# Performance work log

Measured on AMD Instinct MI355X. Metric: run time of the kernel, lower is better.

The kernel has to match this reference:

```python
import jax, jax.numpy as jnp
import numpy as np

EPS = 1e-5

def _batchnorm(h, gamma, beta):
    # training-mode BatchNorm1d over node dim, biased variance
    mu = jnp.mean(h, axis=0)
    var = jnp.mean((h - mu) ** 2, axis=0)
    return (h - mu) * jax.lax.rsqrt(var + EPS) * gamma + beta

def _sage(x, src, dst, n, Wl, b, Wr):
    # sum-aggregate source features into destinations, then linear + root linear
    agg = jax.ops.segment_sum(x[src], dst, num_segments=n)  # [N, F]
    return agg @ Wl + b + x @ Wr

def setup_inputs() -> dict:
    key = jax.random.key(0)
    ks = jax.random.split(key, 8)
    N, E, F, H, O = 200000, 1200000, 64, 128, 128
    s = lambda fan_in: 1.0 / np.sqrt(fan_in)
    return {
        "x": jax.random.normal(ks[0], (N, F), jnp.float32),
        "edge_index": jax.random.randint(ks[1], (2, E), 0, N, jnp.int64),
        "W1l": jax.random.normal(ks[2], (F, H), jnp.float32) * s(F),
        "b1": jnp.zeros((H,), jnp.float32),
        "W1r": jax.random.normal(ks[3], (F, H), jnp.float32) * s(F),
        "g1": jnp.ones((H,), jnp.float32),
        "be1": jnp.zeros((H,), jnp.float32),
        "W2l": jax.random.normal(ks[4], (H, O), jnp.float32) * s(H),
        "b2": jnp.zeros((O,), jnp.float32),
        "W2r": jax.random.normal(ks[5], (H, O), jnp.float32) * s(H),
        "g2": jnp.ones((O,), jnp.float32),
        "be2": jnp.zeros((O,), jnp.float32),
    }

def reference(x, edge_index, W1l, b1, W1r, g1, be1, W2l, b2, W2r, g2, be2):
    n = x.shape[0]
    src, dst = edge_index[0], edge_index[1]
    h = jax.nn.relu(_sage(x, src, dst, n, W1l, b1, W1r))
    h = _batchnorm(h, g1, be1)
    h = jax.nn.relu(_sage(h, src, dst, n, W2l, b2, W2r))
    h = _batchnorm(h, g2, be2)
    return jax.nn.relu(h)
```

## Files before the change

kernel.cpp:

```cpp
#include <hip/hip_runtime.h>

#define N_NODES 200000
#define N_EDGES 1200000
#define F_IN    64
#define F_H     128
#define BN_EPS  1e-5f

typedef short bf16x8 __attribute__((ext_vector_type(8)));
typedef float f32x4  __attribute__((ext_vector_type(4)));
typedef unsigned short us4 __attribute__((ext_vector_type(4)));

__device__ __forceinline__ unsigned short f2bf(float f) {
    union { float f; unsigned u; } v; v.f = f;
    unsigned r = (v.u + 0x7FFFu + ((v.u >> 16) & 1u)) >> 16;
    return (unsigned short)r;
}
__device__ __forceinline__ float bf2f(unsigned short b) {
    union { unsigned u; float f; } v; v.u = ((unsigned)b) << 16;
    return v.f;
}

__global__ void pack_weights_kernel(const float* __restrict__ W,
                                    const float* __restrict__ kscale,
                                    short* __restrict__ P, int KT)
{
    int t = blockIdx.x * 256 + threadIdx.x;
    if (t >= 8 * KT * 64) return;
    int lane = t & 63;
    int kt   = (t >> 6) % KT;
    int nt   = t / (64 * KT);
    int k0   = kt * 32 + (lane >> 4) * 8;
    int n    = nt * 16 + (lane & 15);
#pragma unroll
    for (int j = 0; j < 8; ++j) {
        float w = W[(size_t)(k0 + j) * 128 + n];
        if (kscale) w *= kscale[k0 + j];
        P[(size_t)t * 8 + j] = (short)f2bf(w);
    }
}

__global__ __launch_bounds__(256) void hist_kernel(const int* __restrict__ ei,
                                                   int* __restrict__ deg, int E)
{
    int e = blockIdx.x * 256 + threadIdx.x;
    if (e < E) atomicAdd(&deg[ei[E + e]], 1);
}

__global__ __launch_bounds__(256) void scan1_kernel(const int* __restrict__ deg,
        int* __restrict__ part, int* __restrict__ bsum, int n)
{
    __shared__ int s[256];
    int t = threadIdx.x;
    int base = blockIdx.x * 1024 + t * 4;
    int v[4];
#pragma unroll
    for (int j = 0; j < 4; ++j) v[j] = (base + j < n) ? deg[base + j] : 0;
    int tsum = v[0] + v[1] + v[2] + v[3];
    s[t] = tsum;
    __syncthreads();
    for (int off = 1; off < 256; off <<= 1) {
        int xv = (t >= off) ? s[t - off] : 0;
        __syncthreads();
        s[t] += xv;
        __syncthreads();
    }
    int excl = s[t] - tsum;
#pragma unroll
    for (int j = 0; j < 4; ++j) {
        if (base + j < n) part[base + j] = excl;
        excl += v[j];
    }
    if (t == 255) bsum[blockIdx.x] = s[255];
}

__global__ void scan2_kernel(int* __restrict__ bsum, int nb)
{
    __shared__ int s[256];
    int t = threadIdx.x;
    int v = (t < nb) ? bsum[t] : 0;
    s[t] = v;
    __syncthreads();
    for (int off = 1; off < 256; off <<= 1) {
        int xv = (t >= off) ? s[t - off] : 0;
        __syncthreads();
        s[t] += xv;
        __syncthreads();
    }
    if (t < nb) bsum[t] = s[t] - v;
}

__global__ __launch_bounds__(256) void scan3_kernel(
    const int* __restrict__ part, const int* __restrict__ bsum,
    const int* __restrict__ deg, int* __restrict__ rowptr,
    int* __restrict__ cursor, float* __restrict__ degf, int n, int E)
{
    int i = blockIdx.x * 256 + threadIdx.x;
    if (i == 0) rowptr[n] = E;
    if (i >= n) return;
    int r = part[i] + bsum[i >> 10];
    rowptr[i] = r;
    cursor[i] = r;
    degf[i]   = (float)deg[i];
}

__global__ __launch_bounds__(256) void fill_kernel(const int* __restrict__ ei,
        int* __restrict__ cursor, int* __restrict__ ssrc, int E)
{
    int e = blockIdx.x * 256 + threadIdx.x;
    if (e >= E) return;
    int d = ei[E + e];
    int pos = atomicAdd(&cursor[d], 1);
    ssrc[pos] = ei[e];
}

__global__ __launch_bounds__(256) void gather1_kernel(
    const float* __restrict__ x, const int* __restrict__ rowptr,
    const int* __restrict__ ssrc, unsigned short* __restrict__ aggb)
{
    const int tid  = threadIdx.x;
    const int wv   = tid >> 6;
    const int lane = tid & 63;
    const int sub  = lane >> 4;
    const int li   = lane & 15;
    const int row  = blockIdx.x * 16 + wv * 4 + sub;

    int b = rowptr[row], e = rowptr[row + 1];
    float4 acc = {0.f, 0.f, 0.f, 0.f};
    if (b < e) {
        int s = ssrc[b];
        for (int j = b; j < e; ++j) {
            int sn = (j + 1 < e) ? ssrc[j + 1] : 0;
            float4 v = ((const float4*)(x + (size_t)s * F_IN))[li];
            acc.x += v.x; acc.y += v.y; acc.z += v.z; acc.w += v.w;
            s = sn;
        }
    }
    us4 o;
    o.x = f2bf(acc.x); o.y = f2bf(acc.y); o.z = f2bf(acc.z); o.w = f2bf(acc.w);
    *(us4*)(aggb + (size_t)row * F_IN + li * 4) = o;
}

__global__ __launch_bounds__(256) void gather2_kernel(
    const unsigned short* __restrict__ t1, const int* __restrict__ rowptr,
    const int* __restrict__ ssrc, unsigned short* __restrict__ aggb)
{
    const int tid  = threadIdx.x;
    const int wv   = tid >> 6;
    const int lane = tid & 63;
    const int sub  = lane >> 4;
    const int li   = lane & 15;
    const int row  = blockIdx.x * 16 + wv * 4 + sub;

    int b = rowptr[row], e = rowptr[row + 1];
    float acc[8] = {};
    if (b < e) {
        int s = ssrc[b];
        for (int j = b; j < e; ++j) {
            int sn = (j + 1 < e) ? ssrc[j + 1] : 0;
            bf16x8 v = *(const bf16x8*)(t1 + (size_t)s * F_H + li * 8);
#pragma unroll
            for (int k = 0; k < 8; ++k) acc[k] += bf2f((unsigned short)v[k]);
            s = sn;
        }
    }
    bf16x8 o;
#pragma unroll
    for (int k = 0; k < 8; ++k) o[k] = (short)f2bf(acc[k]);
    *(bf16x8*)(aggb + (size_t)row * F_H + li * 8) = o;
}

template<int K, bool L2>
__global__ __launch_bounds__(256) void gemm_mfma_kernel(
    const unsigned short* __restrict__ Ab,
    const float* __restrict__ Xf,
    const unsigned short* __restrict__ Xb,
    const short* __restrict__ Wlp, const short* __restrict__ Wrp,
    const float* __restrict__ bias,
    const float* __restrict__ c2, const float* __restrict__ degf,
    float* __restrict__ outF, unsigned short* __restrict__ outB,
    float* __restrict__ gsum, float* __restrict__ gsq)
{
    constexpr int KT = K / 32;
    __shared__ float sS[128];
    __shared__ float sQ[128];

    const int tid  = threadIdx.x;
    const int lane = tid & 63;
    const int wv   = tid >> 6;
    const int m    = lane & 15;
    const int quad = lane >> 4;
    const int rowbase = blockIdx.x * 64 + wv * 16;
    const int row  = rowbase + m;

    if (tid < 128) { sS[tid] = 0.f; sQ[tid] = 0.f; }

    f32x4 acc[8] = {};

#pragma unroll
    for (int kt = 0; kt < KT; ++kt) {
        const int k0 = kt * 32 + quad * 8;
        bf16x8 af = *(const bf16x8*)(Ab + (size_t)row * K + k0);
        bf16x8 xf;
        if constexpr (L2) {
            xf = *(const bf16x8*)(Xb + (size_t)row * K + k0);
        } else {
            const float4* xp = (const float4*)(Xf + (size_t)row * K + k0);
            float4 x0 = xp[0], x1 = xp[1];
            xf[0] = (short)f2bf(x0.x); xf[1] = (short)f2bf(x0.y);
            xf[2] = (short)f2bf(x0.z); xf[3] = (short)f2bf(x0.w);
            xf[4] = (short)f2bf(x1.x); xf[5] = (short)f2bf(x1.y);
            xf[6] = (short)f2bf(x1.z); xf[7] = (short)f2bf(x1.w);
        }

#pragma unroll
        for (int nt = 0; nt < 8; ++nt) {
            bf16x8 wl = *(const bf16x8*)(Wlp + ((size_t)(nt * KT + kt) * 64 + lane) * 8);
            acc[nt] = __builtin_amdgcn_mfma_f32_16x16x32_bf16(af, wl, acc[nt], 0, 0, 0);
            bf16x8 wr = *(const bf16x8*)(Wrp + ((size_t)(nt * KT + kt) * 64 + lane) * 8);
            acc[nt] = __builtin_amdgcn_mfma_f32_16x16x32_bf16(xf, wr, acc[nt], 0, 0, 0);
        }
    }

    __syncthreads();

    const int col_l = lane & 15;
    const int orow  = rowbase + quad * 4;
    float dg[4];
    if constexpr (L2) {
#pragma unroll
        for (int r = 0; r < 4; ++r) dg[r] = degf[orow + r];
    }
#pragma unroll
    for (int nt = 0; nt < 8; ++nt) {
        int col = nt * 16 + col_l;
        float b = bias[col];
        float cc = L2 ? c2[col] : 0.f;
        float s = 0.f, q = 0.f;
#pragma unroll
        for (int r = 0; r < 4; ++r) {
            float base = L2 ? fmaf(dg[r], cc, b) : b;
            float v = fmaxf(acc[nt][r] + base, 0.f);
            if constexpr (L2) outF[(size_t)(orow + r) * 128 + col] = v;
            else              outB[(size_t)(orow + r) * 128 + col] = f2bf(v);
            s += v;
            q = fmaf(v, v, q);
        }
        atomicAdd(&sS[col], s);
        atomicAdd(&sQ[col], q);
    }
    __syncthreads();
    if (tid < 128) {
        atomicAdd(&gsum[tid], sS[tid]);
        atomicAdd(&gsq[tid],  sQ[tid]);
    }
}

__global__ void bn_finalize_kernel(
    const float* __restrict__ gsum, const float* __restrict__ gsq,
    const float* __restrict__ g, const float* __restrict__ be,
    float* __restrict__ scale, float* __restrict__ shift, float invN)
{
    int c = threadIdx.x;
    float mean = gsum[c] * invN;
    float var  = fmaxf(gsq[c] * invN - mean * mean, 0.f);
    float sc   = g[c] * rsqrtf(var + BN_EPS);
    scale[c] = sc;
    shift[c] = be[c] - mean * sc;
}

__global__ void bn_fold_kernel(
    const float* __restrict__ shift1, const float* __restrict__ W2l,
    const float* __restrict__ W2r, const float* __restrict__ b2,
    float* __restrict__ c2, float* __restrict__ crb)
{
    int col = threadIdx.x;
    float a = 0.f, r = 0.f;
    for (int k = 0; k < 128; ++k) {
        float s = shift1[k];
        a = fmaf(s, W2l[(size_t)k * 128 + col], a);
        r = fmaf(s, W2r[(size_t)k * 128 + col], r);
    }
    c2[col]  = a;
    crb[col] = r + b2[col];
}

__global__ __launch_bounds__(256) void bn_apply_relu_kernel(
    float* __restrict__ h, const float* __restrict__ scale,
    const float* __restrict__ shift, int n4)
{
    int i = blockIdx.x * 256 + threadIdx.x;
    if (i >= n4) return;
    int cb = i & 31;
    float4 v  = ((float4*)h)[i];
    float4 sc = ((const float4*)scale)[cb];
    float4 sh = ((const float4*)shift)[cb];
    v.x = fmaxf(fmaf(v.x, sc.x, sh.x), 0.f);
    v.y = fmaxf(fmaf(v.y, sc.y, sh.y), 0.f);
    v.z = fmaxf(fmaf(v.z, sc.z, sh.z), 0.f);
    v.w = fmaxf(fmaf(v.w, sc.w, sh.w), 0.f);
    ((float4*)h)[i] = v;
}

extern "C" void kernel_launch(void* const* d_in, const int* in_sizes, int n_in,
                              void* d_out, int out_size, void* d_ws, size_t ws_size,
                              hipStream_t stream) {
    const float* x   = (const float*)d_in[0];
    const int*   ei  = (const int*)d_in[1];
    const float* W1l = (const float*)d_in[2];
    const float* b1  = (const float*)d_in[3];
    const float* W1r = (const float*)d_in[4];
    const float* g1  = (const float*)d_in[5];
    const float* be1 = (const float*)d_in[6];
    const float* W2l = (const float*)d_in[7];
    const float* b2  = (const float*)d_in[8];
    const float* W2r = (const float*)d_in[9];
    const float* g2  = (const float*)d_in[10];
    const float* be2 = (const float*)d_in[11];
    float* out = (float*)d_out;

    const int N = N_NODES, E = N_EDGES;
    const int NB1 = (N + 1023) / 1024;

    float* ws     = (float*)d_ws;
    float* gsum1  = ws;        float* gsq1   = ws + 128;
    float* gsum2  = ws + 256;  float* gsq2   = ws + 384;
    float* scale1 = ws + 512;  float* shift1 = ws + 640;
    float* scale2 = ws + 768;  float* shift2 = ws + 896;
    float* c2v    = ws + 1024; float* crb    = ws + 1152;
    short* W1lp = (short*)(ws + 1536);
    short* W1rp = (short*)(ws + 1536 + 4096);
    short* W2lp = (short*)(ws + 1536 + 8192);
    short* W2rp = (short*)(ws + 1536 + 16384);
    int*   deg    = (int*)(ws + 26112);
    int*   part   = deg + N;
    int*   bsum   = part + N;
    int*   rowptr = bsum + 1024;
    int*   cursor = rowptr + (N + 1024);
    float* degf   = (float*)(cursor + N);
    int*   ssrc   = (int*)(degf + N);
    unsigned short* t1   = (unsigned short*)(ssrc + E);
    unsigned short* aggb = t1 + (size_t)N * F_H;

    hipMemsetAsync(ws, 0, 1024 * sizeof(float), stream);
    hipMemsetAsync(deg, 0, (size_t)N * sizeof(int), stream);
    pack_weights_kernel<<<4, 256, 0, stream>>>(W1l, nullptr, W1lp, 2);
    pack_weights_kernel<<<4, 256, 0, stream>>>(W1r, nullptr, W1rp, 2);
    hist_kernel<<<(E + 255) / 256, 256, 0, stream>>>(ei, deg, E);
    scan1_kernel<<<NB1, 256, 0, stream>>>(deg, part, bsum, N);
    scan2_kernel<<<1, 256, 0, stream>>>(bsum, NB1);
    scan3_kernel<<<(N + 255) / 256, 256, 0, stream>>>(part, bsum, deg, rowptr,
                                                      cursor, degf, N, E);
    fill_kernel<<<(E + 255) / 256, 256, 0, stream>>>(ei, cursor, ssrc, E);

    gather1_kernel<<<N / 16, 256, 0, stream>>>(x, rowptr, ssrc, aggb);
    gemm_mfma_kernel<F_IN, false><<<N / 64, 256, 0, stream>>>(
        aggb, x, nullptr, W1lp, W1rp, b1, nullptr, nullptr,
        nullptr, t1, gsum1, gsq1);
    bn_finalize_kernel<<<1, 128, 0, stream>>>(gsum1, gsq1, g1, be1,
                                              scale1, shift1, 1.f / N);

    pack_weights_kernel<<<8, 256, 0, stream>>>(W2l, scale1, W2lp, 4);
    pack_weights_kernel<<<8, 256, 0, stream>>>(W2r, scale1, W2rp, 4);
    bn_fold_kernel<<<1, 128, 0, stream>>>(shift1, W2l, W2r, b2, c2v, crb);
    gather2_kernel<<<N / 16, 256, 0, stream>>>(t1, rowptr, ssrc, aggb);
    gemm_mfma_kernel<F_H, true><<<N / 64, 256, 0, stream>>>(
        aggb, nullptr, t1, W2lp, W2rp, crb, c2v, degf,
        out, nullptr, gsum2, gsq2);
    bn_finalize_kernel<<<1, 128, 0, stream>>>(gsum2, gsq2, g2, be2,
                                              scale2, shift2, 1.f / N);
    bn_apply_relu_kernel<<<(N * F_H / 4 + 255) / 256, 256, 0, stream>>>(
        out, scale2, shift2, N * F_H / 4);
}
```

Measured before the change: 698.2 us.

## Stage weights in LDS and use persistent grid with 4 row-subtiles per wave

The GEMM kernels now load the packed Wl/Wr weights into shared memory once per block and run as a persistent grid of 512 blocks looping over 256-row tiles. Each wave processes four 16-row subtiles, so every weight fragment feeds four MFMAs. BatchNorm statistics are kept in registers across tiles and flushed to LDS and global atomics once per block. The goal is to cut repeated global weight loads, per-block atomic traffic and launch overhead. In exchange it raises register pressure (128 accumulator floats) and LDS use (up to 64KB for K=128), which may lower occupancy.

```diff
diff --git a/kernel.cpp b/kernel.cpp
--- a/kernel.cpp
+++ b/kernel.cpp
@@ -178,9 +178,11 @@
     const float* __restrict__ bias,
     const float* __restrict__ c2, const float* __restrict__ degf,
     float* __restrict__ outF, unsigned short* __restrict__ outB,
-    float* __restrict__ gsum, float* __restrict__ gsq)
+    float* __restrict__ gsum, float* __restrict__ gsq, int nTiles)
 {
     constexpr int KT = K / 32;
+    constexpr int CH = K * 16;
+    __shared__ bf16x8 wlds[2 * CH];
     __shared__ float sS[128];
     __shared__ float sQ[128];
 
@@ -189,64 +191,99 @@
     const int wv   = tid >> 6;
     const int m    = lane & 15;
     const int quad = lane >> 4;
-    const int rowbase = blockIdx.x * 64 + wv * 16;
-    const int row  = rowbase + m;
-
+    const int col_l = m;
+
+    {
+        const bf16x8* s1 = (const bf16x8*)Wlp;
+        const bf16x8* s2 = (const bf16x8*)Wrp;
+        for (int i = tid; i < CH; i += 256) wlds[i] = s1[i];
+        for (int i = tid; i < CH; i += 256) wlds[CH + i] = s2[i];
+    }
     if (tid < 128) { sS[tid] = 0.f; sQ[tid] = 0.f; }
-
-    f32x4 acc[8] = {};
-
-#pragma unroll
-    for (int kt = 0; kt < KT; ++kt) {
-        const int k0 = kt * 32 + quad * 8;
-        bf16x8 af = *(const bf16x8*)(Ab + (size_t)row * K + k0);
-        bf16x8 xf;
-        if constexpr (L2) {
-            xf = *(const bf16x8*)(Xb + (size_t)row * K + k0);
-        } else {
-            const float4* xp = (const float4*)(Xf + (size_t)row * K + k0);
-            float4 x0 = xp[0], x1 = xp[1];
-            xf[0] = (short)f2bf(x0.x); xf[1] = (short)f2bf(x0.y);
-            xf[2] = (short)f2bf(x0.z); xf[3] = (short)f2bf(x0.w);
-            xf[4] = (short)f2bf(x1.x); xf[5] = (short)f2bf(x1.y);
-            xf[6] = (short)f2bf(x1.z); xf[7] = (short)f2bf(x1.w);
+    __syncthreads();
+
+    float bcol[8], ccol[8];
+#pragma unroll
+    for (int nt = 0; nt < 8; ++nt) {
+        bcol[nt] = bias[nt * 16 + col_l];
+        if constexpr (L2) ccol[nt] = c2[nt * 16 + col_l];
+    }
+
+    float stS[8] = {}, stQ[8] = {};
+
+    for (int tile = blockIdx.x; tile < nTiles; tile += gridDim.x) {
+        const int rowbase = tile * 256 + wv * 64;
+        f32x4 acc[4][8] = {};
+
+#pragma unroll
+        for (int kt = 0; kt < KT; ++kt) {
+            const int k0 = kt * 32 + quad * 8;
+            bf16x8 af[4], xf[4];
+#pragma unroll
+            for (int st = 0; st < 4; ++st) {
+                int r  = rowbase + st * 16 + m;
+                int rc = r < N_NODES ? r : N_NODES - 1;
+                af[st] = *(const bf16x8*)(Ab + (size_t)rc * K + k0);
+                if constexpr (L2) {
+                    xf[st] = *(const bf16x8*)(Xb + (size_t)rc * K + k0);
+                } else {
+                    const float4* xp = (const float4*)(Xf + (size_t)rc * K + k0);
+                    float4 x0 = xp[0], x1 = xp[1];
+                    xf[st][0] = (short)f2bf(x0.x); xf[st][1] = (short)f2bf(x0.y);
+                    xf[st][2] = (short)f2bf(x0.z); xf[st][3] = (short)f2bf(x0.w);
+                    xf[st][4] = (short)f2bf(x1.x); xf[st][5] = (short)f2bf(x1.y);
+                    xf[st][6] = (short)f2bf(x1.z); xf[st][7] = (short)f2bf(x1.w);
+                }
+            }
+#pragma unroll
+            for (int nt = 0; nt < 8; ++nt) {
+                bf16x8 wl = wlds[(nt * KT + kt) * 64 + lane];
+#pragma unroll
+                for (int st = 0; st < 4; ++st)
+                    acc[st][nt] = __builtin_amdgcn_mfma_f32_16x16x32_bf16(
+                        af[st], wl, acc[st][nt], 0, 0, 0);
+                bf16x8 wr = wlds[CH + (nt * KT + kt) * 64 + lane];
+#pragma unroll
+                for (int st = 0; st < 4; ++st)
+                    acc[st][nt] = __builtin_amdgcn_mfma_f32_16x16x32_bf16(
+                        xf[st], wr, acc[st][nt], 0, 0, 0);
+            }
         }
 
 #pragma unroll
-        for (int nt = 0; nt < 8; ++nt) {
-            bf16x8 wl = *(const bf16x8*)(Wlp + ((size_t)(nt * KT + kt) * 64 + lane) * 8);
-            acc[nt] = __builtin_amdgcn_mfma_f32_16x16x32_bf16(af, wl, acc[nt], 0, 0, 0);
-            bf16x8 wr = *(const bf16x8*)(Wrp + ((size_t)(nt * KT + kt) * 64 + lane) * 8);
-            acc[nt] = __builtin_amdgcn_mfma_f32_16x16x32_bf16(xf, wr, acc[nt], 0, 0, 0);
+        for (int st = 0; st < 4; ++st) {
+            const int orow = rowbase + st * 16 + quad * 4;
+            float dg[4];
+            if constexpr (L2) {
+#pragma unroll
+                for (int r = 0; r < 4; ++r) {
+                    int rr = orow + r;
+                    dg[r] = (rr < N_NODES) ? degf[rr] : 0.f;
+                }
+            }
+#pragma unroll
+            for (int nt = 0; nt < 8; ++nt) {
+                int col = nt * 16 + col_l;
+#pragma unroll
+                for (int r = 0; r < 4; ++r) {
+                    int rr = orow + r;
+                    if (rr < N_NODES) {
+                        float base = L2 ? fmaf(dg[r], ccol[nt], bcol[nt]) : bcol[nt];
+                        float v = fmaxf(acc[st][nt][r] + base, 0.f);
+                        if constexpr (L2) outF[(size_t)rr * 128 + col] = v;
+                        else              outB[(size_t)rr * 128 + col] = f2bf(v);
+                        stS[nt] += v;
+                        stQ[nt] = fmaf(v, v, stQ[nt]);
+                    }
+                }
+            }
         }
     }
 
-    __syncthreads();
-
-    const int col_l = lane & 15;
-    const int orow  = rowbase + quad * 4;
-    float dg[4];
-    if constexpr (L2) {
-#pragma unroll
-        for (int r = 0; r < 4; ++r) dg[r] = degf[orow + r];
-    }
 #pragma unroll
     for (int nt = 0; nt < 8; ++nt) {
-        int col = nt * 16 + col_l;
-        float b = bias[col];
-        float cc = L2 ? c2[col] : 0.f;
-        float s = 0.f, q = 0.f;
-#pragma unroll
-        for (int r = 0; r < 4; ++r) {
-            float base = L2 ? fmaf(dg[r], cc, b) : b;
-            float v = fmaxf(acc[nt][r] + base, 0.f);
-            if constexpr (L2) outF[(size_t)(orow + r) * 128 + col] = v;
-            else              outB[(size_t)(orow + r) * 128 + col] = f2bf(v);
-            s += v;
-            q = fmaf(v, v, q);
-        }
-        atomicAdd(&sS[col], s);
-        atomicAdd(&sQ[col], q);
+        atomicAdd(&sS[nt * 16 + col_l], stS[nt]);
+        atomicAdd(&sQ[nt * 16 + col_l], stQ[nt]);
     }
     __syncthreads();
     if (tid < 128) {
@@ -320,6 +357,7 @@
 
     const int N = N_NODES, E = N_EDGES;
     const int NB1 = (N + 1023) / 1024;
+    const int nTiles = (N + 255) / 256;
 
     float* ws     = (float*)d_ws;
     float* gsum1  = ws;        float* gsq1   = ws + 128;
@@ -353,9 +391,9 @@
     fill_kernel<<<(E + 255) / 256, 256, 0, stream>>>(ei, cursor, ssrc, E);
 
     gather1_kernel<<<N / 16, 256, 0, stream>>>(x, rowptr, ssrc, aggb);
-    gemm_mfma_kernel<F_IN, false><<<N / 64, 256, 0, stream>>>(
+    gemm_mfma_kernel<F_IN, false><<<512, 256, 0, stream>>>(
         aggb, x, nullptr, W1lp, W1rp, b1, nullptr, nullptr,
-        nullptr, t1, gsum1, gsq1);
+        nullptr, t1, gsum1, gsq1, nTiles);
     bn_finalize_kernel<<<1, 128, 0, stream>>>(gsum1, gsq1, g1, be1,
                                               scale1, shift1, 1.f / N);
 
@@ -363,9 +401,9 @@
     pack_weights_kernel<<<8, 256, 0, stream>>>(W2r, scale1, W2rp, 4);
     bn_fold_kernel<<<1, 128, 0, stream>>>(shift1, W2l, W2r, b2, c2v, crb);
     gather2_kernel<<<N / 16, 256, 0, stream>>>(t1, rowptr, ssrc, aggb);
-    gemm_mfma_kernel<F_H, true><<<N / 64, 256, 0, stream>>>(
+    gemm_mfma_kernel<F_H, true><<<512, 256, 0, stream>>>(
         aggb, nullptr, t1, W2lp, W2rp, crb, c2v, degf,
-        out, nullptr, gsum2, gsq2);
+        out, nullptr, gsum2, gsq2, nTiles);
     bn_finalize_kernel<<<1, 128, 0, stream>>>(gsum2, gsq2, g2, be2,
                                               scale2, shift2, 1.f / N);
     bn_apply_relu_kernel<<<(N * F_H / 4 + 255) / 256, 256, 0, stream>>>(
```

After: 632.9 us. 9.4% less time.
